# Optimization experiments

Hardware: AMD Instinct MI355X
Metric: run time of the kernel (lower is better)

The kernel has to match this reference:

```python
import jax, jax.numpy as jnp
import numpy as np

EPS_NORM = 1e-12   # F.normalize eps
EPS_SCALE = 1e-5   # activation scale clamp


def _weight_quant(w):
    # ternary (sign) quantization with mean-abs scale
    scale = jnp.mean(jnp.abs(w))
    u = jnp.sign(w - jnp.mean(w))
    return u, scale


def _activation_quant(x):
    # SimpleRMSNorm: l2-normalize over last dim, times dim**-0.5
    dim_scale = x.shape[-1] ** -0.5
    l2 = jnp.linalg.norm(x, axis=-1, keepdims=True)
    xn = x / jnp.maximum(l2, EPS_NORM) * dim_scale
    # per-token int8 scale
    scale = 127.0 / jnp.maximum(jnp.max(jnp.abs(xn), axis=-1, keepdims=True), EPS_SCALE)
    y = jnp.clip(jnp.round(xn * scale), -128.0, 127.0)
    return y, scale


def setup_inputs() -> dict:
    key = jax.random.key(0)
    kx, kw, kb = jax.random.split(key, 3)
    B, S, D, O = 4, 8192, 1024, 1024
    x = jax.random.normal(kx, (B, S, D), dtype=jnp.float32)
    w = jax.random.normal(kw, (O, D), dtype=jnp.float32)
    b = jax.random.normal(kb, (O,), dtype=jnp.float32)
    return {"x": x, "w": w, "b": b}


def reference(x, w, b):
    w_q, w_scale = _weight_quant(w)          # [O,D], scalar
    b_q, b_scale = _weight_quant(b)          # [O], scalar
    x_q, x_scale = _activation_quant(x)      # [B,S,D], [B,S,1]
    # mm + broadcast bias add, then dequant by product of all three scales
    y = jnp.einsum('bsd,od->bso', x_q, w_q) + b_q
    return y / (w_scale * x_scale * b_scale)
```

## Files before the change

### kernel.cpp

```cpp
#include <hip/hip_runtime.h>
#include <cstdint>
#include <cstddef>


typedef __attribute__((ext_vector_type(4))) int int4v;

static constexpr int DIM = 1024;
static constexpr int OUTF = 1024;
static constexpr int MROWS = 32768;
static constexpr float INV_WN = 1.0f / (1024.0f * 1024.0f);
static constexpr float INV_BN = 1.0f / 1024.0f;

#define OFF_XSCALE 1024
#define OFF_WQ 132096
#define OFF_XQ 1180672

__device__ inline float wave_sum(float v) {
#pragma unroll
  for (int off = 32; off; off >>= 1) v += __shfl_xor(v, off);
  return v;
}
__device__ inline float wave_max(float v) {
#pragma unroll
  for (int off = 32; off; off >>= 1) v = fmaxf(v, __shfl_xor(v, off));
  return v;
}

__global__ __launch_bounds__(256) void reduce_wb(const float* __restrict__ w,
                                                 const float* __restrict__ b,
                                                 float* __restrict__ red) {
  __shared__ float ss[4], sa[4];
  const int t = threadIdx.x;
  const int lane = t & 63, wv = t >> 6;
  float s = 0.0f, a = 0.0f;
  const float4* w4 = (const float4*)w;
  const int idx = blockIdx.x * 256 + t;
#pragma unroll
  for (int i = 0; i < 4; ++i) {
    float4 v = w4[idx + i * 65536];
    s += (v.x + v.y) + (v.z + v.w);
    a += (fabsf(v.x) + fabsf(v.y)) + (fabsf(v.z) + fabsf(v.w));
  }
  s = wave_sum(s);
  a = wave_sum(a);
  if (lane == 0) { ss[wv] = s; sa[wv] = a; }
  __syncthreads();
  if (t == 0) atomicAdd(&red[0], (ss[0] + ss[1]) + (ss[2] + ss[3]));
  if (t == 1) atomicAdd(&red[1], (sa[0] + sa[1]) + (sa[2] + sa[3]));
  if (blockIdx.x == 0) {
    __syncthreads();
    float4 v = ((const float4*)b)[t];
    float s2 = (v.x + v.y) + (v.z + v.w);
    float a2 = (fabsf(v.x) + fabsf(v.y)) + (fabsf(v.z) + fabsf(v.w));
    s2 = wave_sum(s2);
    a2 = wave_sum(a2);
    if (lane == 0) { ss[wv] = s2; sa[wv] = a2; }
    __syncthreads();
    if (t == 0) {
      red[2] = (ss[0] + ss[1]) + (ss[2] + ss[3]);
      red[3] = (sa[0] + sa[1]) + (sa[2] + sa[3]);
    }
  }
}

__global__ __launch_bounds__(256) void quant_w(const float* __restrict__ w,
                                               const float* __restrict__ red,
                                               signed char* __restrict__ wq) {
  const float wmean = red[0] * INV_WN;
  const int idx = blockIdx.x * 256 + threadIdx.x;
  float4 v = ((const float4*)w)[idx];
  int q0, q1, q2, q3;
  float d;
  d = v.x - wmean; q0 = d > 0.f ? 1 : (d < 0.f ? -1 : 0);
  d = v.y - wmean; q1 = d > 0.f ? 1 : (d < 0.f ? -1 : 0);
  d = v.z - wmean; q2 = d > 0.f ? 1 : (d < 0.f ? -1 : 0);
  d = v.w - wmean; q3 = d > 0.f ? 1 : (d < 0.f ? -1 : 0);
  const int pk = (q0 & 0xff) | ((q1 & 0xff) << 8) | ((q2 & 0xff) << 16) | ((q3 & 0xff) << 24);
  ((int*)wq)[idx] = pk;
}

__global__ __launch_bounds__(256) void quant_x(const float* __restrict__ x,
                                               signed char* __restrict__ xq,
                                               float* __restrict__ xscale) {
  const int wv = threadIdx.x >> 6;
  const int lane = threadIdx.x & 63;
  const int row = blockIdx.x * 4 + wv;
  const float4* xr = (const float4*)(x + (size_t)row * DIM);
  float4 v[4];
  float ss = 0.0f, ma = 0.0f;
#pragma unroll
  for (int it = 0; it < 4; ++it) {
    v[it] = xr[it * 64 + lane];
    ss += v[it].x * v[it].x + v[it].y * v[it].y + v[it].z * v[it].z + v[it].w * v[it].w;
    ma = fmaxf(ma, fmaxf(fmaxf(fabsf(v[it].x), fabsf(v[it].y)),
                         fmaxf(fabsf(v[it].z), fabsf(v[it].w))));
  }
  ss = wave_sum(ss);
  ma = wave_max(ma);

  const float l2 = sqrtf(ss);
  const float inv = 0.03125f / fmaxf(l2, 1e-12f);
  const float scale = 127.0f / fmaxf(ma * inv, 1e-5f);
  const float f = inv * scale;

  int* outp = (int*)(xq + (size_t)row * DIM);
#pragma unroll
  for (int it = 0; it < 4; ++it) {
    const int q0 = (int)fminf(fmaxf(rintf(v[it].x * f), -128.f), 127.f);
    const int q1 = (int)fminf(fmaxf(rintf(v[it].y * f), -128.f), 127.f);
    const int q2 = (int)fminf(fmaxf(rintf(v[it].z * f), -128.f), 127.f);
    const int q3 = (int)fminf(fmaxf(rintf(v[it].w * f), -128.f), 127.f);
    outp[it * 64 + lane] =
        (q0 & 0xff) | ((q1 & 0xff) << 8) | ((q2 & 0xff) << 16) | ((q3 & 0xff) << 24);
  }
  if (lane == 0) xscale[row] = scale;
}

__global__ __launch_bounds__(512, 2) void gemm_i8(
    const signed char* __restrict__ Aq,
    const signed char* __restrict__ Wq,
    const float* __restrict__ bias,
    const float* __restrict__ red,
    const float* __restrict__ xscale,
    float* __restrict__ out) {
  __shared__ signed char As[2][256 * 128];
  __shared__ signed char Bs[2][256 * 128];

  const int t = threadIdx.x;
  const int lane = t & 63;
  const int wv = t >> 6;
  const int quad = lane >> 4;
  const int r16 = lane & 15;
  const int wr = wv >> 2;
  const int wc = wv & 3;

  const int orig = blockIdx.x;
  const int swz = (orig & 7) * 64 + (orig >> 3);
  const int bn = swz & 3;
  const int bm = swz >> 2;

  const signed char* Ab = Aq + (size_t)bm * 256 * DIM;
  const signed char* Bb = Wq + (size_t)bn * 256 * DIM;

  const int ldsoff = lane * 16;
  const int row8 = lane >> 3;
  const int sw16 = (((lane & 7) ^ row8) << 4);

  int4v acc[8][4] = {};

#define STAGE(tt, dd)                                                            \
  do {                                                                           \
    const size_t koff_ = (size_t)(tt) * 128 + sw16;                              \
    _Pragma("unroll") for (int i_ = 0; i_ < 4; ++i_) {                           \
      const int blk_ = wv * 4 + i_;              \
      const size_t roff_ = (size_t)(blk_ * 8 + row8) * DIM + koff_;              \
      __builtin_amdgcn_global_load_lds(                                          \
          (const __attribute__((address_space(1))) void*)(Ab + roff_),           \
          (__attribute__((address_space(3))) void*)(&As[dd][blk_ * 1024 + ldsoff]), \
          16, 0, 0);                                                             \
      __builtin_amdgcn_global_load_lds(                                          \
          (const __attribute__((address_space(1))) void*)(Bb + roff_),           \
          (__attribute__((address_space(3))) void*)(&Bs[dd][blk_ * 1024 + ldsoff]), \
          16, 0, 0);                                                             \
    }                                                                            \
  } while (0)

#define COMPUTE(cc)                                                              \
  do {                                                                           \
    const int swr_ = (r16 & 7) << 4;                                             \
    int4v bf[4][2];                                                              \
    _Pragma("unroll") for (int j_ = 0; j_ < 4; ++j_) {                           \
      const int r_ = wc * 64 + j_ * 16 + r16;                                    \
      _Pragma("unroll") for (int s_ = 0; s_ < 2; ++s_)                           \
          bf[j_][s_] = *(const int4v*)&Bs[cc][r_ * 128 +                         \
                                              ((s_ * 64 + quad * 16) ^ swr_)];   \
    }                                                                            \
    _Pragma("unroll") for (int mq_ = 0; mq_ < 2; ++mq_) {                        \
      int4v af[4][2];                                                            \
      _Pragma("unroll") for (int i_ = 0; i_ < 4; ++i_) {                         \
        const int r_ = wr * 128 + mq_ * 64 + i_ * 16 + r16;                      \
        _Pragma("unroll") for (int s_ = 0; s_ < 2; ++s_)                         \
            af[i_][s_] = *(const int4v*)&As[cc][r_ * 128 +                       \
                                                ((s_ * 64 + quad * 16) ^ swr_)]; \
      }                                                                          \
      asm volatile("s_barrier" ::: "memory");                                    \
      __builtin_amdgcn_s_setprio(1);                                             \
      _Pragma("unroll") for (int i_ = 0; i_ < 4; ++i_)                           \
          _Pragma("unroll") for (int j_ = 0; j_ < 4; ++j_) {                     \
        acc[mq_ * 4 + i_][j_] = __builtin_amdgcn_mfma_i32_16x16x64_i8(           \
            af[i_][0], bf[j_][0], acc[mq_ * 4 + i_][j_], 0, 0, 0);               \
        acc[mq_ * 4 + i_][j_] = __builtin_amdgcn_mfma_i32_16x16x64_i8(           \
            af[i_][1], bf[j_][1], acc[mq_ * 4 + i_][j_], 0, 0, 0);               \
      }                                                                          \
      __builtin_amdgcn_s_setprio(0);                                             \
      asm volatile("s_barrier" ::: "memory");                                    \
    }                                                                            \
  } while (0)

  STAGE(0, 0);
#pragma unroll 1
  for (int tp = 0; tp < 4; ++tp) {
    STAGE(2 * tp + 1, 1);
    asm volatile("s_waitcnt vmcnt(8)" ::: "memory");
    asm volatile("s_barrier" ::: "memory");
    COMPUTE(0);
    if (tp < 3) {
      STAGE(2 * tp + 2, 0);
      asm volatile("s_waitcnt vmcnt(8)" ::: "memory");
    } else {
      asm volatile("s_waitcnt vmcnt(0)" ::: "memory");
    }
    asm volatile("s_barrier" ::: "memory");
    COMPUTE(1);
  }
#undef COMPUTE
#undef STAGE

  const float wscale = red[1] * INV_WN;
  const float bscale = red[3] * INV_BN;
  const float bmean = red[2] * INV_BN;
  const float wb = wscale * bscale;

  int bq[4];
#pragma unroll
  for (int j = 0; j < 4; ++j) {
    const float bd = bias[bn * 256 + wc * 64 + j * 16 + r16] - bmean;
    bq[j] = bd > 0.f ? 1 : (bd < 0.f ? -1 : 0);
  }

#pragma unroll
  for (int i = 0; i < 8; ++i) {
    const int mg = bm * 256 + wr * 128 + i * 16 + quad * 4;
    float rec[4];
#pragma unroll
    for (int rr = 0; rr < 4; ++rr) rec[rr] = 1.0f / (wb * xscale[mg + rr]);
#pragma unroll
    for (int j = 0; j < 4; ++j) {
      float* po = out + (size_t)mg * OUTF + bn * 256 + wc * 64 + j * 16 + r16;
#pragma unroll
      for (int rr = 0; rr < 4; ++rr)
        po[(size_t)rr * OUTF] = (float)(acc[i][j][rr] + bq[j]) * rec[rr];
    }
  }
}

extern "C" void kernel_launch(void* const* d_in, const int* in_sizes, int n_in,
                              void* d_out, int out_size, void* d_ws, size_t ws_size,
                              hipStream_t stream) {
  const float* x = (const float*)d_in[0];
  const float* w = (const float*)d_in[1];
  const float* b = (const float*)d_in[2];
  float* out = (float*)d_out;
  char* ws = (char*)d_ws;

  float* red = (float*)ws;
  float* xscale = (float*)(ws + OFF_XSCALE);
  signed char* wq = (signed char*)(ws + OFF_WQ);
  signed char* xq = (signed char*)(ws + OFF_XQ);

  hipMemsetAsync(red, 0, 4 * sizeof(float), stream);
  reduce_wb<<<256, 256, 0, stream>>>(w, b, red);
  quant_w<<<1024, 256, 0, stream>>>(w, red, wq);
  quant_x<<<MROWS / 4, 256, 0, stream>>>(x, xq, xscale);
  gemm_i8<<<dim3(512), 512, 0, stream>>>(xq, wq, b, red, xscale, out);
}
```

Before: 293.3 us.

## Switch int8 GEMM to 32x32x32 MFMA tiles with per-tile barriers removed

Result: faster. 285.0 us (-2.8%).

```diff
diff --git a/kernel.cpp b/kernel.cpp
--- a/kernel.cpp
+++ b/kernel.cpp
@@ -4,6 +4,7 @@
 
 
 typedef __attribute__((ext_vector_type(4))) int int4v;
+typedef __attribute__((ext_vector_type(16))) int int16v;
 
 static constexpr int DIM = 1024;
 static constexpr int OUTF = 1024;
@@ -129,8 +130,8 @@
   const int t = threadIdx.x;
   const int lane = t & 63;
   const int wv = t >> 6;
-  const int quad = lane >> 4;
-  const int r16 = lane & 15;
+  const int l31 = lane & 31;
+  const int hi = lane >> 5;
   const int wr = wv >> 2;
   const int wc = wv & 3;
 
@@ -146,7 +147,7 @@
   const int row8 = lane >> 3;
   const int sw16 = (((lane & 7) ^ row8) << 4);
 
-  int4v acc[8][4] = {};
+  int16v acc[4][2] = {};
 
 #define STAGE(tt, dd)                                                            \
   do {                                                                           \
@@ -167,33 +168,26 @@
 
 #define COMPUTE(cc)                                                              \
   do {                                                                           \
-    const int swr_ = (r16 & 7) << 4;                                             \
-    int4v bf[4][2];                                                              \
-    _Pragma("unroll") for (int j_ = 0; j_ < 4; ++j_) {                           \
-      const int r_ = wc * 64 + j_ * 16 + r16;                                    \
-      _Pragma("unroll") for (int s_ = 0; s_ < 2; ++s_)                           \
-          bf[j_][s_] = *(const int4v*)&Bs[cc][r_ * 128 +                         \
-                                              ((s_ * 64 + quad * 16) ^ swr_)];   \
+    const int swr_ = (lane & 7) << 4;      \
+    int4v bf[2][4];                                                              \
+    _Pragma("unroll") for (int nf_ = 0; nf_ < 2; ++nf_) {                        \
+      const int r_ = wc * 64 + nf_ * 32 + l31;                                   \
+      _Pragma("unroll") for (int ks_ = 0; ks_ < 4; ++ks_)                        \
+          bf[nf_][ks_] = *(const int4v*)&Bs[cc][r_ * 128 +                       \
+                                                ((ks_ * 32 + hi * 16) ^ swr_)];  \
     }                                                                            \
-    _Pragma("unroll") for (int mq_ = 0; mq_ < 2; ++mq_) {                        \
-      int4v af[4][2];                                                            \
-      _Pragma("unroll") for (int i_ = 0; i_ < 4; ++i_) {                         \
-        const int r_ = wr * 128 + mq_ * 64 + i_ * 16 + r16;                      \
-        _Pragma("unroll") for (int s_ = 0; s_ < 2; ++s_)                         \
-            af[i_][s_] = *(const int4v*)&As[cc][r_ * 128 +                       \
-                                                ((s_ * 64 + quad * 16) ^ swr_)]; \
-      }                                                                          \
-      asm volatile("s_barrier" ::: "memory");                                    \
+    _Pragma("unroll") for (int mf_ = 0; mf_ < 4; ++mf_) {                        \
+      int4v af[4];                                                               \
+      const int r_ = wr * 128 + mf_ * 32 + l31;                                  \
+      _Pragma("unroll") for (int ks_ = 0; ks_ < 4; ++ks_)                        \
+          af[ks_] = *(const int4v*)&As[cc][r_ * 128 +                            \
+                                           ((ks_ * 32 + hi * 16) ^ swr_)];       \
       __builtin_amdgcn_s_setprio(1);                                             \
-      _Pragma("unroll") for (int i_ = 0; i_ < 4; ++i_)                           \
-          _Pragma("unroll") for (int j_ = 0; j_ < 4; ++j_) {                     \
-        acc[mq_ * 4 + i_][j_] = __builtin_amdgcn_mfma_i32_16x16x64_i8(           \
-            af[i_][0], bf[j_][0], acc[mq_ * 4 + i_][j_], 0, 0, 0);               \
-        acc[mq_ * 4 + i_][j_] = __builtin_amdgcn_mfma_i32_16x16x64_i8(           \
-            af[i_][1], bf[j_][1], acc[mq_ * 4 + i_][j_], 0, 0, 0);               \
-      }                                                                          \
+      _Pragma("unroll") for (int nf_ = 0; nf_ < 2; ++nf_)                        \
+          _Pragma("unroll") for (int ks_ = 0; ks_ < 4; ++ks_)                    \
+              acc[mf_][nf_] = __builtin_amdgcn_mfma_i32_32x32x32_i8(             \
+                  af[ks_], bf[nf_][ks_], acc[mf_][nf_], 0, 0, 0);                \
       __builtin_amdgcn_s_setprio(0);                                             \
-      asm volatile("s_barrier" ::: "memory");                                    \
     }                                                                            \
   } while (0)
 
@@ -204,6 +198,7 @@
     asm volatile("s_waitcnt vmcnt(8)" ::: "memory");
     asm volatile("s_barrier" ::: "memory");
     COMPUTE(0);
+    asm volatile("s_barrier" ::: "memory");
     if (tp < 3) {
       STAGE(2 * tp + 2, 0);
       asm volatile("s_waitcnt vmcnt(8)" ::: "memory");
@@ -212,6 +207,7 @@
     }
     asm volatile("s_barrier" ::: "memory");
     COMPUTE(1);
+    asm volatile("s_barrier" ::: "memory");
   }
 #undef COMPUTE
 #undef STAGE
@@ -221,25 +217,34 @@
   const float bmean = red[2] * INV_BN;
   const float wb = wscale * bscale;
 
-  int bq[4];
-#pragma unroll
-  for (int j = 0; j < 4; ++j) {
-    const float bd = bias[bn * 256 + wc * 64 + j * 16 + r16] - bmean;
-    bq[j] = bd > 0.f ? 1 : (bd < 0.f ? -1 : 0);
-  }
-
-#pragma unroll
-  for (int i = 0; i < 8; ++i) {
-    const int mg = bm * 256 + wr * 128 + i * 16 + quad * 4;
-    float rec[4];
-#pragma unroll
-    for (int rr = 0; rr < 4; ++rr) rec[rr] = 1.0f / (wb * xscale[mg + rr]);
-#pragma unroll
-    for (int j = 0; j < 4; ++j) {
-      float* po = out + (size_t)mg * OUTF + bn * 256 + wc * 64 + j * 16 + r16;
-#pragma unroll
-      for (int rr = 0; rr < 4; ++rr)
-        po[(size_t)rr * OUTF] = (float)(acc[i][j][rr] + bq[j]) * rec[rr];
+  int bq[2];
+#pragma unroll
+  for (int nf = 0; nf < 2; ++nf) {
+    const float bd = bias[bn * 256 + wc * 64 + nf * 32 + l31] - bmean;
+    bq[nf] = bd > 0.f ? 1 : (bd < 0.f ? -1 : 0);
+  }
+
+#pragma unroll
+  for (int mf = 0; mf < 4; ++mf) {
+#pragma unroll
+    for (int rq = 0; rq < 4; ++rq) {
+      const int mg = bm * 256 + wr * 128 + mf * 32 + rq * 8 + hi * 4;
+      const float4 xs = *(const float4*)&xscale[mg];
+      float rec[4];
+      rec[0] = 1.0f / (wb * xs.x);
+      rec[1] = 1.0f / (wb * xs.y);
+      rec[2] = 1.0f / (wb * xs.z);
+      rec[3] = 1.0f / (wb * xs.w);
+#pragma unroll
+      for (int nf = 0; nf < 2; ++nf) {
+        const int n = bn * 256 + wc * 64 + nf * 32 + l31;
+#pragma unroll
+        for (int rr = 0; rr < 4; ++rr) {
+          const int reg = rq * 4 + rr;
+          out[(size_t)(mg + rr) * OUTF + n] =
+              (float)(acc[mf][nf][reg] + bq[nf]) * rec[rr];
+        }
+      }
     }
   }
 }
```
